# Kernel optimization log

Measured on AMD Instinct MI355X. Metric: run time of the kernel, lower is better.

Reference implementation:

```python
import jax, jax.numpy as jnp
import numpy as np

N, E, G = 50000, 800000, 500
IN_DIM, EXTRA, HID, HEADS, NCLS = 128, 32, 64, 4, 1
NODE_FEAT2 = HID * HEADS  # 256, input to layer 2
FINAL = NODE_FEAT2 + EXTRA
NODES_PER_GRAPH = N // G  # 100


def gat_layer(h, W, a_l, a_r, b, src, dst, internal_relu):
    # DGL GATConv: fc -> per-head attn logits -> leaky_relu -> edge softmax (over dst) -> weighted sum
    feat = (h @ W).reshape(N, HEADS, HID)            # [N,H,D]
    el = jnp.sum(feat * a_l, axis=-1)                # [N,H]
    er = jnp.sum(feat * a_r, axis=-1)                # [N,H]
    e = jax.nn.leaky_relu(el[src] + er[dst], negative_slope=0.2)  # [E,H]
    m = jax.ops.segment_max(e, dst, num_segments=N)  # [N,H] (stable softmax)
    ex = jnp.exp(e - m[dst])
    denom = jax.ops.segment_sum(ex, dst, num_segments=N)
    alpha = ex / denom[dst]                          # [E,H]
    msg = feat[src] * alpha[:, :, None]              # [E,H,D]
    rst = jax.ops.segment_sum(msg, dst, num_segments=N) + b.reshape(1, HEADS, HID)
    if internal_relu:
        rst = jax.nn.relu(rst)
    return rst


def setup_inputs() -> dict:
    key = jax.random.key(0)
    ks = jax.random.split(key, 20)
    s = 0.05
    inp = {
        "x": jax.random.normal(ks[0], (N, IN_DIM), jnp.float32),
        "desc": jax.random.normal(ks[1], (G, EXTRA), jnp.float32),
        "src": jax.random.randint(ks[2], (E,), 0, N, jnp.int32),
        "dst": jax.random.randint(ks[3], (E,), 0, N, jnp.int32),
        "graph_id": (jnp.arange(N) // NODES_PER_GRAPH).astype(jnp.int32),
        # layer 1 params
        "W1": jax.random.normal(ks[4], (IN_DIM, HEADS * HID), jnp.float32) * s,
        "al1": jax.random.normal(ks[5], (HEADS, HID), jnp.float32) * s,
        "ar1": jax.random.normal(ks[6], (HEADS, HID), jnp.float32) * s,
        "b1": jnp.zeros((HEADS * HID,), jnp.float32),
        # layer 2 params
        "W2": jax.random.normal(ks[7], (NODE_FEAT2, HEADS * HID), jnp.float32) * s,
        "al2": jax.random.normal(ks[8], (HEADS, HID), jnp.float32) * s,
        "ar2": jax.random.normal(ks[9], (HEADS, HID), jnp.float32) * s,
        "b2": jnp.zeros((HEADS * HID,), jnp.float32),
        # MLP head (weights stored [in,out])
        "fc1_w": jax.random.normal(ks[10], (FINAL, HID), jnp.float32) * s,
        "fc1_b": jnp.zeros((HID,), jnp.float32),
        "fc2_w": jax.random.normal(ks[11], (HID, HID // 2), jnp.float32) * s,
        "fc2_b": jnp.zeros((HID // 2,), jnp.float32),
        "out_w": jax.random.normal(ks[12], (HID // 2, NCLS), jnp.float32) * s,
        "out_b": jnp.zeros((NCLS,), jnp.float32),
    }
    return inp


def reference(x, desc, src, dst, graph_id, W1, al1, ar1, b1, W2, al2, ar2, b2,
              fc1_w, fc1_b, fc2_w, fc2_b, out_w, out_b):
    h = gat_layer(x, W1, al1, ar1, b1, src, dst, internal_relu=True)
    h = jax.nn.relu(h.reshape(N, -1))                # flatten heads + outer relu (dropout=0)
    h = gat_layer(h, W2, al2, ar2, b2, src, dst, internal_relu=False)
    h = jax.nn.relu(h.reshape(N, -1))
    # dgl.mean_nodes over batched graph
    hg = jax.ops.segment_sum(h, graph_id, num_segments=G) / float(NODES_PER_GRAPH)  # [G, 256]
    combined = jnp.concatenate([hg, desc], axis=1)   # [G, 288]
    z = jax.nn.relu(combined @ fc1_w + fc1_b)
    z = jax.nn.relu(z @ fc2_w + fc2_b)
    return z @ out_w + out_b                          # [G, 1]
```

## Files before the change

### kernel.cpp

```cpp
#include <hip/hip_runtime.h>
#include <hip/hip_bf16.h>

#define N_NODES 50000
#define N_EDGES 800000
#define N_GRAPHS 500
#define IN_DIM 128
#define EXTRA 32
#define HID 64
#define HEADS 4
#define F2 256
#define NODES_PER_GRAPH 100
#define SCAN_BLOCKS ((N_NODES + 1023) / 1024)

typedef unsigned short u16;
typedef __attribute__((ext_vector_type(8))) short short8;
typedef __attribute__((ext_vector_type(4))) float floatx4;

__device__ __forceinline__ float bf2f(u16 u) {
    union { unsigned int i; float f; } v;
    v.i = ((unsigned int)u) << 16;
    return v.f;
}
__device__ __forceinline__ u16 f2b(float f) {
    __hip_bfloat16 h = __float2bfloat16(f);
    return *reinterpret_cast<u16*>(&h);
}

#define CNT_BLK 3125
#define CVT_BLK 6250
#define RP1_BLK 16
#define RP2_BLK 32
__global__ __launch_bounds__(256) void prep_kernel(const int* __restrict__ dst,
                                                   int* __restrict__ cnt,
                                                   const float* __restrict__ x,
                                                   u16* __restrict__ xb,
                                                   const float* __restrict__ W1,
                                                   u16* __restrict__ BF1,
                                                   const float* __restrict__ W2,
                                                   u16* __restrict__ BF2) {
    int b = blockIdx.x, t = threadIdx.x;
    if (b < CNT_BLK) {
        int e = b * 256 + t;
        if (e < N_EDGES) atomicAdd(&cnt[dst[e]], 1);
    } else if (b < CNT_BLK + CVT_BLK) {
        int i = (b - CNT_BLK) * 256 + t;
        float4 v = reinterpret_cast<const float4*>(x)[i];
        ushort4 o;
        o.x = f2b(v.x); o.y = f2b(v.y); o.z = f2b(v.z); o.w = f2b(v.w);
        reinterpret_cast<ushort4*>(xb)[i] = o;
    } else {
        const float* W;
        u16* BF;
        int chunk;
        if (b < CNT_BLK + CVT_BLK + RP1_BLK) {
            W = W1; BF = BF1; chunk = (b - CNT_BLK - CVT_BLK) * 4 + (t >> 6);
        } else {
            W = W2; BF = BF2; chunk = (b - CNT_BLK - CVT_BLK - RP1_BLK) * 4 + (t >> 6);
        }
        int l = t & 63;
        int kt = chunk >> 4, ct = chunk & 15;
        int col = ct * 16 + (l & 15);
        int k0 = kt * 32 + 8 * (l >> 4);
        u16* p = BF + (size_t)chunk * 512 + l * 8;
#pragma unroll
        for (int j = 0; j < 8; ++j) p[j] = f2b(W[(size_t)(k0 + j) * 256 + col]);
    }
}

__global__ __launch_bounds__(1024) void scan_block_kernel(const int* __restrict__ cnt,
                                                          int* __restrict__ part,
                                                          int* __restrict__ bsum) {
    __shared__ int buf[1024];
    int b = blockIdx.x, t = threadIdx.x;
    int i = b * 1024 + t;
    buf[t] = (i < N_NODES) ? cnt[i] : 0;
    __syncthreads();
    for (int d = 1; d < 1024; d <<= 1) {
        int add = (t >= d) ? buf[t - d] : 0;
        __syncthreads();
        buf[t] += add;
        __syncthreads();
    }
    if (i < N_NODES) part[i] = buf[t];
    if (t == 1023) bsum[b] = buf[t];
}

__global__ __launch_bounds__(1024) void scan_finalize_kernel(const int* __restrict__ part,
                                                             const int* __restrict__ bsum,
                                                             int* __restrict__ offs) {
    __shared__ int sbase;
    int t = threadIdx.x;
    if (t < 64) {
        int v = (t < blockIdx.x) ? bsum[t] : 0;
#pragma unroll
        for (int d = 32; d > 0; d >>= 1) v += __shfl_xor(v, d);
        if (t == 0) sbase = v;
    }
    __syncthreads();
    int i = blockIdx.x * 1024 + t;
    if (i < N_NODES) {
        offs[i + 1] = part[i] + sbase;
        if (i == 0) offs[0] = 0;
    }
}

__global__ void scatter_w_kernel(const int* __restrict__ src, const int* __restrict__ dst,
                                 const int* __restrict__ offs, int* __restrict__ fill,
                                 int* __restrict__ csr_src, int* __restrict__ pos_arr,
                                 const float* __restrict__ el, const float* __restrict__ er,
                                 float* __restrict__ w) {
    int e = blockIdx.x * blockDim.x + threadIdx.x;
    if (e >= N_EDGES) return;
    int s = src[e], d = dst[e];
    int pos = offs[d] + atomicAdd(&fill[d], 1);
    csr_src[pos] = s;
    pos_arr[e] = pos;
    float4 l = *reinterpret_cast<const float4*>(&el[s * 4]);
    float4 r = *reinterpret_cast<const float4*>(&er[d * 4]);
    float4 o; float v;
    v = l.x + r.x; v = (v > 0.f) ? v : 0.2f * v; o.x = __expf(v);
    v = l.y + r.y; v = (v > 0.f) ? v : 0.2f * v; o.y = __expf(v);
    v = l.z + r.z; v = (v > 0.f) ? v : 0.2f * v; o.z = __expf(v);
    v = l.w + r.w; v = (v > 0.f) ? v : 0.2f * v; o.w = __expf(v);
    *reinterpret_cast<float4*>(&w[(size_t)pos * 4]) = o;
}

__global__ void edge_w_kernel(const int* __restrict__ src, const int* __restrict__ dst,
                              const int* __restrict__ pos_arr,
                              const float* __restrict__ el, const float* __restrict__ er,
                              float* __restrict__ w) {
    int e = blockIdx.x * blockDim.x + threadIdx.x;
    if (e >= N_EDGES) return;
    int s = src[e], d = dst[e], p = pos_arr[e];
    float4 l = *reinterpret_cast<const float4*>(&el[s * 4]);
    float4 r = *reinterpret_cast<const float4*>(&er[d * 4]);
    float4 o; float v;
    v = l.x + r.x; v = (v > 0.f) ? v : 0.2f * v; o.x = __expf(v);
    v = l.y + r.y; v = (v > 0.f) ? v : 0.2f * v; o.y = __expf(v);
    v = l.z + r.z; v = (v > 0.f) ? v : 0.2f * v; o.z = __expf(v);
    v = l.w + r.w; v = (v > 0.f) ? v : 0.2f * v; o.w = __expf(v);
    *reinterpret_cast<float4*>(&w[(size_t)p * 4]) = o;
}

template <int K>
__global__ __launch_bounds__(256) void gemm_mfma_attn_kernel(const u16* __restrict__ A,
                                                             const u16* __restrict__ BF,
                                                             const float* __restrict__ al,
                                                             const float* __restrict__ ar,
                                                             u16* __restrict__ C,
                                                             float* __restrict__ el,
                                                             float* __restrict__ er, int M) {
    const int NKT = K / 32;
    __shared__ u16 cxpose[4][16 * 68];
    int t = threadIdx.x;
    int wave = t >> 6, lane = t & 63;
    int l15 = lane & 15, kg = lane >> 4;
    int h = wave;
    int ct0 = h * 4;

    short8 breg[NKT][4];
#pragma unroll
    for (int kt = 0; kt < NKT; ++kt)
#pragma unroll
        for (int c = 0; c < 4; ++c)
            breg[kt][c] = *reinterpret_cast<const short8*>(
                              BF + (size_t)(kt * 16 + ct0 + c) * 512 + lane * 8);

    float alv[4], arv[4];
#pragma unroll
    for (int c = 0; c < 4; ++c) {
        alv[c] = al[(ct0 + c) * 16 + l15];
        arv[c] = ar[(ct0 + c) * 16 + l15];
    }

    u16* cbuf = cxpose[wave];
    for (int rt = 0; rt < 4; ++rt) {
        int row0 = blockIdx.x * 64 + rt * 16;
        if (row0 >= M) break;
        int arow = row0 + l15; if (arow >= M) arow = M - 1;
        const u16* Ap = A + (size_t)arow * K + kg * 8;

        floatx4 acc[4];
#pragma unroll
        for (int c = 0; c < 4; ++c) acc[c] = (floatx4)0.0f;
#pragma unroll
        for (int kt = 0; kt < NKT; ++kt) {
            short8 a = *reinterpret_cast<const short8*>(Ap + kt * 32);
#pragma unroll
            for (int c = 0; c < 4; ++c)
                acc[c] = __builtin_amdgcn_mfma_f32_16x16x32_bf16(a, breg[kt][c], acc[c], 0, 0, 0);
        }

        floatx4 pl = (floatx4)0.0f, pr = (floatx4)0.0f;
#pragma unroll
        for (int c = 0; c < 4; ++c) {
            pl += acc[c] * alv[c];
            pr += acc[c] * arv[c];
        }
#pragma unroll
        for (int off = 1; off < 16; off <<= 1) {
#pragma unroll
            for (int j = 0; j < 4; ++j) {
                pl[j] += __shfl_xor(pl[j], off);
                pr[j] += __shfl_xor(pr[j], off);
            }
        }
        if (l15 == 0) {
#pragma unroll
            for (int j = 0; j < 4; ++j) {
                int n = row0 + kg * 4 + j;
                if (n < M) { el[n * 4 + h] = pl[j]; er[n * 4 + h] = pr[j]; }
            }
        }

#pragma unroll
        for (int c = 0; c < 4; ++c)
#pragma unroll
            for (int j = 0; j < 4; ++j)
                cbuf[(kg * 4 + j) * 68 + c * 16 + l15] = f2b(acc[c][j]);
#pragma unroll
        for (int it = 0; it < 2; ++it) {
            int r = (lane >> 3) + it * 8;
            int cg = lane & 7;
            int grow = row0 + r;
            if (grow < M) {
                short8 v = *reinterpret_cast<const short8*>(cbuf + r * 68 + cg * 8);
                *reinterpret_cast<short8*>(C + (size_t)grow * 256 + h * 64 + cg * 8) = v;
            }
        }
    }
}

__global__ __launch_bounds__(256) void gather_kernel(const u16* __restrict__ feat,
                                                     const float* __restrict__ w,
                                                     const int* __restrict__ offs,
                                                     const int* __restrict__ csr_src,
                                                     const float* __restrict__ bias,
                                                     u16* __restrict__ outb) {
    int n = blockIdx.x * 4 + (threadIdx.x >> 6);
    if (n >= N_NODES) return;
    int lane = threadIdx.x & 63;
    int h = lane >> 4;
    const ushort4* feat4 = reinterpret_cast<const ushort4*>(feat);
    int s0 = offs[n], s1 = offs[n + 1];
    float4 acc = make_float4(0.f, 0.f, 0.f, 0.f);
    float den = 0.f;
    int i = s0;
    for (; i + 4 <= s1; i += 4) {
        int n0 = csr_src[i], n1 = csr_src[i + 1], n2 = csr_src[i + 2], n3 = csr_src[i + 3];
        float x0 = w[(size_t)(i + 0) * 4 + h];
        float x1 = w[(size_t)(i + 1) * 4 + h];
        float x2 = w[(size_t)(i + 2) * 4 + h];
        float x3 = w[(size_t)(i + 3) * 4 + h];
        ushort4 f0 = feat4[(size_t)n0 * 64 + lane];
        ushort4 f1 = feat4[(size_t)n1 * 64 + lane];
        ushort4 f2 = feat4[(size_t)n2 * 64 + lane];
        ushort4 f3 = feat4[(size_t)n3 * 64 + lane];
        acc.x = fmaf(x0, bf2f(f0.x), acc.x); acc.y = fmaf(x0, bf2f(f0.y), acc.y);
        acc.z = fmaf(x0, bf2f(f0.z), acc.z); acc.w = fmaf(x0, bf2f(f0.w), acc.w);
        acc.x = fmaf(x1, bf2f(f1.x), acc.x); acc.y = fmaf(x1, bf2f(f1.y), acc.y);
        acc.z = fmaf(x1, bf2f(f1.z), acc.z); acc.w = fmaf(x1, bf2f(f1.w), acc.w);
        acc.x = fmaf(x2, bf2f(f2.x), acc.x); acc.y = fmaf(x2, bf2f(f2.y), acc.y);
        acc.z = fmaf(x2, bf2f(f2.z), acc.z); acc.w = fmaf(x2, bf2f(f2.w), acc.w);
        acc.x = fmaf(x3, bf2f(f3.x), acc.x); acc.y = fmaf(x3, bf2f(f3.y), acc.y);
        acc.z = fmaf(x3, bf2f(f3.z), acc.z); acc.w = fmaf(x3, bf2f(f3.w), acc.w);
        den += (x0 + x1) + (x2 + x3);
    }
    for (; i < s1; ++i) {
        int s = csr_src[i];
        float x = w[(size_t)i * 4 + h];
        ushort4 f = feat4[(size_t)s * 64 + lane];
        acc.x = fmaf(x, bf2f(f.x), acc.x); acc.y = fmaf(x, bf2f(f.y), acc.y);
        acc.z = fmaf(x, bf2f(f.z), acc.z); acc.w = fmaf(x, bf2f(f.w), acc.w);
        den += x;
    }
    float inv = (s1 > s0) ? 1.f / den : 0.f;
    float4 bv = reinterpret_cast<const float4*>(bias)[lane];
    ushort4 o;
    o.x = f2b(fmaxf(fmaf(acc.x, inv, bv.x), 0.f));
    o.y = f2b(fmaxf(fmaf(acc.y, inv, bv.y), 0.f));
    o.z = f2b(fmaxf(fmaf(acc.z, inv, bv.z), 0.f));
    o.w = f2b(fmaxf(fmaf(acc.w, inv, bv.w), 0.f));
    reinterpret_cast<ushort4*>(outb)[(size_t)n * 64 + lane] = o;
}

__global__ __launch_bounds__(256) void head_kernel(const u16* __restrict__ h2,
                                                   const float* __restrict__ desc,
                                                   const float* __restrict__ fc1_w,
                                                   const float* __restrict__ fc1_b,
                                                   const float* __restrict__ fc2_w,
                                                   const float* __restrict__ fc2_b,
                                                   const float* __restrict__ out_w,
                                                   const float* __restrict__ out_b,
                                                   float* __restrict__ out) {
    __shared__ float comb[288];
    __shared__ float z1[64];
    __shared__ float z2[32];
    int g = blockIdx.x, t = threadIdx.x;
    const u16* base = h2 + (size_t)g * NODES_PER_GRAPH * 256;
    float s0 = 0.f, s1 = 0.f, s2 = 0.f, s3 = 0.f;
    for (int i = 0; i < NODES_PER_GRAPH; i += 4) {
        s0 += bf2f(base[(size_t)(i + 0) * 256 + t]);
        s1 += bf2f(base[(size_t)(i + 1) * 256 + t]);
        s2 += bf2f(base[(size_t)(i + 2) * 256 + t]);
        s3 += bf2f(base[(size_t)(i + 3) * 256 + t]);
    }
    comb[t] = ((s0 + s1) + (s2 + s3)) * (1.f / NODES_PER_GRAPH);
    if (t < EXTRA) comb[256 + t] = desc[g * EXTRA + t];
    __syncthreads();
    if (t < 64) {
        float a = fc1_b[t];
        for (int i = 0; i < 288; ++i) a += comb[i] * fc1_w[i * 64 + t];
        z1[t] = fmaxf(a, 0.f);
    }
    __syncthreads();
    if (t < 32) {
        float a = fc2_b[t];
        for (int i = 0; i < 64; ++i) a += z1[i] * fc2_w[i * 32 + t];
        z2[t] = fmaxf(a, 0.f);
    }
    __syncthreads();
    if (t == 0) {
        float a = out_b[0];
        for (int i = 0; i < 32; ++i) a += z2[i] * out_w[i];
        out[g] = a;
    }
}

extern "C" void kernel_launch(void* const* d_in, const int* in_sizes, int n_in,
                              void* d_out, int out_size, void* d_ws, size_t ws_size,
                              hipStream_t stream) {
    const float* x     = (const float*)d_in[0];
    const float* desc  = (const float*)d_in[1];
    const int*   src   = (const int*)d_in[2];
    const int*   dst   = (const int*)d_in[3];
    const float* W1    = (const float*)d_in[5];
    const float* al1   = (const float*)d_in[6];
    const float* ar1   = (const float*)d_in[7];
    const float* b1    = (const float*)d_in[8];
    const float* W2    = (const float*)d_in[9];
    const float* al2   = (const float*)d_in[10];
    const float* ar2   = (const float*)d_in[11];
    const float* b2    = (const float*)d_in[12];
    const float* fc1_w = (const float*)d_in[13];
    const float* fc1_b = (const float*)d_in[14];
    const float* fc2_w = (const float*)d_in[15];
    const float* fc2_b = (const float*)d_in[16];
    const float* out_w = (const float*)d_in[17];
    const float* out_b = (const float*)d_in[18];
    float* out = (float*)d_out;

    char* ws = (char*)d_ws;
    size_t off = 0;
    auto alloc = [&](size_t bytes) -> void* {
        void* p = ws + off;
        off = (off + bytes + 255) & ~(size_t)255;
        return p;
    };
    u16*   xb      = (u16*)alloc((size_t)N_NODES * IN_DIM * 2);
    u16*   featb   = (u16*)alloc((size_t)N_NODES * 256 * 2);
    u16*   h1b     = (u16*)alloc((size_t)N_NODES * 256 * 2);
    u16*   h2b     = (u16*)alloc((size_t)N_NODES * 256 * 2);
    u16*   BF1     = (u16*)alloc((size_t)IN_DIM * 256 * 2);
    u16*   BF2     = (u16*)alloc((size_t)F2 * 256 * 2);
    float* el      = (float*)alloc((size_t)N_NODES * 4 * 4);
    float* er      = (float*)alloc((size_t)N_NODES * 4 * 4);
    int*   offs    = (int*)alloc((size_t)(N_NODES + 1) * 4);
    int*   cntfill = (int*)alloc((size_t)2 * N_NODES * 4);
    int*   part    = (int*)alloc((size_t)N_NODES * 4);
    int*   bsum    = (int*)alloc(64 * 4);
    int*   csr_src = (int*)alloc((size_t)N_EDGES * 4);
    int*   pos_arr = (int*)alloc((size_t)N_EDGES * 4);
    float* wbuf    = (float*)alloc((size_t)N_EDGES * 4 * 4);
    int* cnt = cntfill, *fill = cntfill + N_NODES;

    hipMemsetAsync(cntfill, 0, (size_t)2 * N_NODES * 4, stream);
    prep_kernel<<<CNT_BLK + CVT_BLK + RP1_BLK + RP2_BLK, 256, 0, stream>>>(
        dst, cnt, x, xb, W1, BF1, W2, BF2);
    scan_block_kernel<<<SCAN_BLOCKS, 1024, 0, stream>>>(cnt, part, bsum);
    scan_finalize_kernel<<<SCAN_BLOCKS, 1024, 0, stream>>>(part, bsum, offs);

    int gb = (N_NODES + 63) / 64;
    int eb = (N_EDGES + 255) / 256;
    int ngb = (N_NODES + 3) / 4;
    gemm_mfma_attn_kernel<IN_DIM><<<gb, 256, 0, stream>>>(xb, BF1, al1, ar1, featb, el, er, N_NODES);
    scatter_w_kernel<<<eb, 256, 0, stream>>>(src, dst, offs, fill, csr_src, pos_arr,
                                             el, er, wbuf);
    gather_kernel<<<ngb, 256, 0, stream>>>(featb, wbuf, offs, csr_src, b1, h1b);
    gemm_mfma_attn_kernel<F2><<<gb, 256, 0, stream>>>(h1b, BF2, al2, ar2, featb, el, er, N_NODES);
    edge_w_kernel<<<eb, 256, 0, stream>>>(src, dst, pos_arr, el, er, wbuf);
    gather_kernel<<<ngb, 256, 0, stream>>>(featb, wbuf, offs, csr_src, b2, h2b);
    head_kernel<<<N_GRAPHS, 256, 0, stream>>>(h2b, desc, fc1_w, fc1_b, fc2_w, fc2_b,
                                              out_w, out_b, out);
}
```

Measured before the change: 291.6 us.

## Split gather across column slices with edge-parallel lanes and head-major weights

The CSR scatter is separated from edge-weight computation, which now runs in CSR order using a stored csr_dst array and writes weights head-major. The gather kernel is rewritten so that each wave handles one 32-column slice of a node, with 16 edges in flight per iteration (4 lanes per edge, 8 bf16 each), and the partial results are combined with shuffle reductions. This targets higher memory-level parallelism for low-degree nodes and coalesced weight reads. In exchange it launches eight times more blocks, which reread offsets and csr_src per slice, and adds shuffle-reduction overhead.

After: 480.1 us. 1.65x slower.

```diff
diff --git a/kernel.cpp b/kernel.cpp
--- a/kernel.cpp
+++ b/kernel.cpp
@@ -104,42 +104,30 @@
     }
 }
 
-__global__ void scatter_w_kernel(const int* __restrict__ src, const int* __restrict__ dst,
-                                 const int* __restrict__ offs, int* __restrict__ fill,
-                                 int* __restrict__ csr_src, int* __restrict__ pos_arr,
-                                 const float* __restrict__ el, const float* __restrict__ er,
-                                 float* __restrict__ w) {
+__global__ void scatter_kernel(const int* __restrict__ src, const int* __restrict__ dst,
+                               const int* __restrict__ offs, int* __restrict__ fill,
+                               int* __restrict__ csr_src, int* __restrict__ csr_dst) {
     int e = blockIdx.x * blockDim.x + threadIdx.x;
     if (e >= N_EDGES) return;
     int s = src[e], d = dst[e];
     int pos = offs[d] + atomicAdd(&fill[d], 1);
     csr_src[pos] = s;
-    pos_arr[e] = pos;
+    csr_dst[pos] = d;
+}
+
+__global__ void edge_w_kernel(const int* __restrict__ csr_src, const int* __restrict__ csr_dst,
+                              const float* __restrict__ el, const float* __restrict__ er,
+                              float* __restrict__ w) {
+    int p = blockIdx.x * blockDim.x + threadIdx.x;
+    if (p >= N_EDGES) return;
+    int s = csr_src[p], d = csr_dst[p];
     float4 l = *reinterpret_cast<const float4*>(&el[s * 4]);
     float4 r = *reinterpret_cast<const float4*>(&er[d * 4]);
-    float4 o; float v;
-    v = l.x + r.x; v = (v > 0.f) ? v : 0.2f * v; o.x = __expf(v);
-    v = l.y + r.y; v = (v > 0.f) ? v : 0.2f * v; o.y = __expf(v);
-    v = l.z + r.z; v = (v > 0.f) ? v : 0.2f * v; o.z = __expf(v);
-    v = l.w + r.w; v = (v > 0.f) ? v : 0.2f * v; o.w = __expf(v);
-    *reinterpret_cast<float4*>(&w[(size_t)pos * 4]) = o;
-}
-
-__global__ void edge_w_kernel(const int* __restrict__ src, const int* __restrict__ dst,
-                              const int* __restrict__ pos_arr,
-                              const float* __restrict__ el, const float* __restrict__ er,
-                              float* __restrict__ w) {
-    int e = blockIdx.x * blockDim.x + threadIdx.x;
-    if (e >= N_EDGES) return;
-    int s = src[e], d = dst[e], p = pos_arr[e];
-    float4 l = *reinterpret_cast<const float4*>(&el[s * 4]);
-    float4 r = *reinterpret_cast<const float4*>(&er[d * 4]);
-    float4 o; float v;
-    v = l.x + r.x; v = (v > 0.f) ? v : 0.2f * v; o.x = __expf(v);
-    v = l.y + r.y; v = (v > 0.f) ? v : 0.2f * v; o.y = __expf(v);
-    v = l.z + r.z; v = (v > 0.f) ? v : 0.2f * v; o.z = __expf(v);
-    v = l.w + r.w; v = (v > 0.f) ? v : 0.2f * v; o.w = __expf(v);
-    *reinterpret_cast<float4*>(&w[(size_t)p * 4]) = o;
+    float v;
+    v = l.x + r.x; v = (v > 0.f) ? v : 0.2f * v; w[0 * N_EDGES + p] = __expf(v);
+    v = l.y + r.y; v = (v > 0.f) ? v : 0.2f * v; w[1 * N_EDGES + p] = __expf(v);
+    v = l.z + r.z; v = (v > 0.f) ? v : 0.2f * v; w[2 * N_EDGES + p] = __expf(v);
+    v = l.w + r.w; v = (v > 0.f) ? v : 0.2f * v; w[3 * N_EDGES + p] = __expf(v);
 }
 
 template <int K>
@@ -237,51 +225,47 @@
                                                      const int* __restrict__ csr_src,
                                                      const float* __restrict__ bias,
                                                      u16* __restrict__ outb) {
-    int n = blockIdx.x * 4 + (threadIdx.x >> 6);
+    int slice = blockIdx.x;
+    int n = blockIdx.y * 4 + (threadIdx.x >> 6);
     if (n >= N_NODES) return;
-    int lane = threadIdx.x & 63;
-    int h = lane >> 4;
-    const ushort4* feat4 = reinterpret_cast<const ushort4*>(feat);
+    int j = threadIdx.x & 63;
+    int eslot = j >> 2;
+    int cpos = j & 3;
+    int coff = slice * 32 + cpos * 8;
+    const float* wp = w + (size_t)(slice >> 1) * N_EDGES;
     int s0 = offs[n], s1 = offs[n + 1];
-    float4 acc = make_float4(0.f, 0.f, 0.f, 0.f);
+    float acc[8] = {0.f, 0.f, 0.f, 0.f, 0.f, 0.f, 0.f, 0.f};
     float den = 0.f;
-    int i = s0;
-    for (; i + 4 <= s1; i += 4) {
-        int n0 = csr_src[i], n1 = csr_src[i + 1], n2 = csr_src[i + 2], n3 = csr_src[i + 3];
-        float x0 = w[(size_t)(i + 0) * 4 + h];
-        float x1 = w[(size_t)(i + 1) * 4 + h];
-        float x2 = w[(size_t)(i + 2) * 4 + h];
-        float x3 = w[(size_t)(i + 3) * 4 + h];
-        ushort4 f0 = feat4[(size_t)n0 * 64 + lane];
-        ushort4 f1 = feat4[(size_t)n1 * 64 + lane];
-        ushort4 f2 = feat4[(size_t)n2 * 64 + lane];
-        ushort4 f3 = feat4[(size_t)n3 * 64 + lane];
-        acc.x = fmaf(x0, bf2f(f0.x), acc.x); acc.y = fmaf(x0, bf2f(f0.y), acc.y);
-        acc.z = fmaf(x0, bf2f(f0.z), acc.z); acc.w = fmaf(x0, bf2f(f0.w), acc.w);
-        acc.x = fmaf(x1, bf2f(f1.x), acc.x); acc.y = fmaf(x1, bf2f(f1.y), acc.y);
-        acc.z = fmaf(x1, bf2f(f1.z), acc.z); acc.w = fmaf(x1, bf2f(f1.w), acc.w);
-        acc.x = fmaf(x2, bf2f(f2.x), acc.x); acc.y = fmaf(x2, bf2f(f2.y), acc.y);
-        acc.z = fmaf(x2, bf2f(f2.z), acc.z); acc.w = fmaf(x2, bf2f(f2.w), acc.w);
-        acc.x = fmaf(x3, bf2f(f3.x), acc.x); acc.y = fmaf(x3, bf2f(f3.y), acc.y);
-        acc.z = fmaf(x3, bf2f(f3.z), acc.z); acc.w = fmaf(x3, bf2f(f3.w), acc.w);
-        den += (x0 + x1) + (x2 + x3);
-    }
-    for (; i < s1; ++i) {
-        int s = csr_src[i];
-        float x = w[(size_t)i * 4 + h];
-        ushort4 f = feat4[(size_t)s * 64 + lane];
-        acc.x = fmaf(x, bf2f(f.x), acc.x); acc.y = fmaf(x, bf2f(f.y), acc.y);
-        acc.z = fmaf(x, bf2f(f.z), acc.z); acc.w = fmaf(x, bf2f(f.w), acc.w);
+    for (int i = s0; i < s1; i += 16) {
+        int e = i + eslot;
+        float x = 0.f;
+        short8 f = (short8)0;
+        if (e < s1) {
+            int sn = csr_src[e];
+            x = wp[e];
+            f = *reinterpret_cast<const short8*>(feat + (size_t)sn * 256 + coff);
+        }
+#pragma unroll
+        for (int q = 0; q < 8; ++q) acc[q] = fmaf(x, bf2f((u16)f[q]), acc[q]);
         den += x;
     }
-    float inv = (s1 > s0) ? 1.f / den : 0.f;
-    float4 bv = reinterpret_cast<const float4*>(bias)[lane];
-    ushort4 o;
-    o.x = f2b(fmaxf(fmaf(acc.x, inv, bv.x), 0.f));
-    o.y = f2b(fmaxf(fmaf(acc.y, inv, bv.y), 0.f));
-    o.z = f2b(fmaxf(fmaf(acc.z, inv, bv.z), 0.f));
-    o.w = f2b(fmaxf(fmaf(acc.w, inv, bv.w), 0.f));
-    reinterpret_cast<ushort4*>(outb)[(size_t)n * 64 + lane] = o;
+#pragma unroll
+    for (int off = 4; off < 64; off <<= 1) {
+#pragma unroll
+        for (int q = 0; q < 8; ++q) acc[q] += __shfl_xor(acc[q], off);
+        den += __shfl_xor(den, off);
+    }
+    if (eslot == 0) {
+        float inv = (s1 > s0) ? 1.f / den : 0.f;
+        float4 bv0 = *reinterpret_cast<const float4*>(&bias[coff]);
+        float4 bv1 = *reinterpret_cast<const float4*>(&bias[coff + 4]);
+        float bb[8] = {bv0.x, bv0.y, bv0.z, bv0.w, bv1.x, bv1.y, bv1.z, bv1.w};
+        short8 o;
+#pragma unroll
+        for (int q = 0; q < 8; ++q)
+            o[q] = (short)f2b(fmaxf(fmaf(acc[q], inv, bb[q]), 0.f));
+        *reinterpret_cast<short8*>(outb + (size_t)n * 256 + coff) = o;
+    }
 }
 
 __global__ __launch_bounds__(256) void head_kernel(const u16* __restrict__ h2,
@@ -370,8 +354,8 @@
     int*   part    = (int*)alloc((size_t)N_NODES * 4);
     int*   bsum    = (int*)alloc(64 * 4);
     int*   csr_src = (int*)alloc((size_t)N_EDGES * 4);
-    int*   pos_arr = (int*)alloc((size_t)N_EDGES * 4);
-    float* wbuf    = (float*)alloc((size_t)N_EDGES * 4 * 4);
+    int*   csr_dst = (int*)alloc((size_t)N_EDGES * 4);
+    float* wbuf    = (float*)alloc((size_t)4 * N_EDGES * 4);
     int* cnt = cntfill, *fill = cntfill + N_NODES;
 
     hipMemsetAsync(cntfill, 0, (size_t)2 * N_NODES * 4, stream);
@@ -379,17 +363,18 @@
         dst, cnt, x, xb, W1, BF1, W2, BF2);
     scan_block_kernel<<<SCAN_BLOCKS, 1024, 0, stream>>>(cnt, part, bsum);
     scan_finalize_kernel<<<SCAN_BLOCKS, 1024, 0, stream>>>(part, bsum, offs);
+    scatter_kernel<<<(N_EDGES + 255) / 256, 256, 0, stream>>>(src, dst, offs, fill,
+                                                              csr_src, csr_dst);
 
     int gb = (N_NODES + 63) / 64;
     int eb = (N_EDGES + 255) / 256;
-    int ngb = (N_NODES + 3) / 4;
+    dim3 ng(8, (N_NODES + 3) / 4);
     gemm_mfma_attn_kernel<IN_DIM><<<gb, 256, 0, stream>>>(xb, BF1, al1, ar1, featb, el, er, N_NODES);
-    scatter_w_kernel<<<eb, 256, 0, stream>>>(src, dst, offs, fill, csr_src, pos_arr,
-                                             el, er, wbuf);
-    gather_kernel<<<ngb, 256, 0, stream>>>(featb, wbuf, offs, csr_src, b1, h1b);
+    edge_w_kernel<<<eb, 256, 0, stream>>>(csr_src, csr_dst, el, er, wbuf);
+    gather_kernel<<<ng, 256, 0, stream>>>(featb, wbuf, offs, csr_src, b1, h1b);
     gemm_mfma_attn_kernel<F2><<<gb, 256, 0, stream>>>(h1b, BF2, al2, ar2, featb, el, er, N_NODES);
-    edge_w_kernel<<<eb, 256, 0, stream>>>(src, dst, pos_arr, el, er, wbuf);
-    gather_kernel<<<ngb, 256, 0, stream>>>(featb, wbuf, offs, csr_src, b2, h2b);
+    edge_w_kernel<<<eb, 256, 0, stream>>>(csr_src, csr_dst, el, er, wbuf);
+    gather_kernel<<<ng, 256, 0, stream>>>(featb, wbuf, offs, csr_src, b2, h2b);
     head_kernel<<<N_GRAPHS, 256, 0, stream>>>(h2b, desc, fc1_w, fc1_b, fc2_w, fc2_b,
                                               out_w, out_b, out);
 }
```
